# Kernel tuning notes

Hardware: AMD Instinct MI355X
Metric: run time of the kernel (lower is better)

Reference implementation:

```python
import jax, jax.numpy as jnp
import numpy as np

D = 768       # input_dim / model width
H = 3072      # expert hidden width (init arg 'output_dim')
E = 8         # num_experts
K = 2         # top_k
NOISE_STD = 0.1
B, S = 2, 1024


def setup_inputs() -> dict:
    key = jax.random.key(0)
    ks = jax.random.split(key, 16)
    sd = lambda fan_in: 1.0 / np.sqrt(fan_in)
    return {
        "x": jax.random.normal(ks[0], (B, S, D), dtype=jnp.float32),
        "noise": jax.random.normal(ks[1], (B, S, E), dtype=jnp.float32),
        # router
        "Wr": jax.random.normal(ks[2], (D, E), dtype=jnp.float32) * sd(D),
        "br": jnp.zeros((E,), dtype=jnp.float32),
        # stacked expert FFNs: d -> h -> d
        "W1": jax.random.normal(ks[3], (E, D, H), dtype=jnp.float32) * sd(D),
        "b1": jnp.zeros((E, H), dtype=jnp.float32),
        "W2": jax.random.normal(ks[4], (E, H, D), dtype=jnp.float32) * sd(H),
        "b2": jnp.zeros((E, D), dtype=jnp.float32),
        # shared expert
        "Ws1": jax.random.normal(ks[5], (D, H), dtype=jnp.float32) * sd(D),
        "bs1": jnp.zeros((H,), dtype=jnp.float32),
        "Ws2": jax.random.normal(ks[6], (H, D), dtype=jnp.float32) * sd(H),
        "bs2": jnp.zeros((D,), dtype=jnp.float32),
        # mixing scalars (alpha trainable, beta frozen in torch)
        "alpha": jnp.float32(0.3),
        "beta": jnp.float32(0.7),
    }


def reference(x, noise, Wr, br, W1, b1, W2, b2, Ws1, bs1, Ws2, bs2, alpha, beta):
    b, s, d = x.shape
    xt = x.reshape(-1, d)                       # [T, D]
    nt = noise.reshape(-1, E)                   # [T, E]
    T = xt.shape[0]

    # router: noisy logits -> top-k -> softmax over selected experts only
    logits = xt @ Wr + br + NOISE_STD * nt      # [T, E]
    top_vals, top_idx = jax.lax.top_k(logits, K)  # [T, K]
    top_w = jax.nn.softmax(top_vals, axis=-1)     # softmax over -inf-masked logits == softmax over top-k
    gates = jnp.zeros((T, E), dtype=x.dtype).at[jnp.arange(T)[:, None], top_idx].set(top_w)  # [T, E], 0 elsewhere

    # experts (dense over E; non-selected contributions are zeroed by gates)
    h = jax.nn.leaky_relu(jnp.einsum('td,edh->teh', xt, W1) + b1, negative_slope=0.01)  # [T, E, H]
    y = jnp.einsum('teh,ehd->ted', h, W2) + b2                                          # [T, E, D]
    moe_out = jnp.einsum('ted,te->td', y, gates)                                        # [T, D]

    # shared expert
    sh = jax.nn.leaky_relu(xt @ Ws1 + bs1, negative_slope=0.01)
    shared_out = sh @ Ws2 + bs2                                                         # [T, D]

    w = jax.nn.softmax(jnp.stack([alpha, beta]))
    out = shared_out * w[0] + moe_out * w[1]
    return out.reshape(b, s, d)
```

## Files before the change

kernel.cpp:

```cpp
#include <hip/hip_runtime.h>
#include <hip/hip_bf16.h>
#include <cstdio>
#include <cstdint>

#define TNUM 2048
#define DDIM 768
#define HDIM 3072
#define ENUM 8

#define WAITVM(N) asm volatile("s_waitcnt vmcnt(" #N ")" ::: "memory")
#define MEMFENCE() asm volatile("" ::: "memory")

typedef __attribute__((ext_vector_type(8))) __bf16 bf16x8;
typedef __attribute__((ext_vector_type(4))) float f32x4;

__device__ __forceinline__ unsigned short f2bf(float f) {
    __bf16 h = (__bf16)f;
    unsigned short u;
    __builtin_memcpy(&u, &h, 2);
    return u;
}

__device__ __forceinline__ void async_cp16(const unsigned short* g, unsigned short* l) {
    __builtin_amdgcn_global_load_lds((const __attribute__((address_space(1))) void*)g,
                                     (__attribute__((address_space(3))) void*)l,
                                     16, 0, 0);
}

__device__ __forceinline__ void transpose_tile(const float* __restrict__ in,
                                               unsigned short* __restrict__ out,
                                               int R, int C, int c0, int r0,
                                               unsigned int* tileT32) {
    int tid = threadIdx.x;
    int l15 = tid & 15;
    int g = tid >> 4;
    int par = (g >> 1) & 1;
    int hf = g & 1;
    int cb = hf * 64 + l15 * 4;
    const float* src = in + (size_t)(r0 + (g >> 1)) * C + c0 + cb;
    float4 v[16];
    #pragma unroll
    for (int p = 0; p < 16; p++)
        v[p] = *(const float4*)(src + (size_t)p * 8 * C);
    #pragma unroll
    for (int p = 0; p < 16; p++) {
        int unit = p * 16 + g;
        unsigned int m01 = (unsigned int)f2bf(v[p].x) | ((unsigned int)f2bf(v[p].y) << 16);
        unsigned int m23 = (unsigned int)f2bf(v[p].z) | ((unsigned int)f2bf(v[p].w) << 16);
        unsigned int o01 = __shfl_xor(m01, 32);
        unsigned int o23 = __shfl_xor(m23, 32);
        unsigned int wA = par ? ((o23 & 0xffffu) | (m23 << 16))
                              : ((m01 & 0xffffu) | (o01 << 16));
        unsigned int wB = par ? ((o23 >> 16) | (m23 & 0xffff0000u))
                              : ((m01 >> 16) | (o01 & 0xffff0000u));
        int ca = cb + par * 2;
        int rp = unit >> 2;
        int cq = ca >> 2;
        int woff = 4 * (((rp >> 2) + 3 * cq) & 15) + (((rp & 3) + cq) & 3);
        tileT32[ca * 68 + woff] = wA;
        tileT32[(ca + 1) * 68 + woff] = wB;
    }
    __syncthreads();
    uint4 Wv[8];
    #pragma unroll
    for (int p = 0; p < 8; p++) {
        int cc = p * 16 + g;
        int cqp = cc >> 2;
        Wv[p] = *(const uint4*)&tileT32[cc * 68 + 4 * ((l15 + 3 * cqp) & 15)];
    }
    #pragma unroll
    for (int p = 0; p < 8; p++) {
        int cc = p * 16 + g;
        int cqp = cc >> 2;
        unsigned int a0 = Wv[p].x, a1 = Wv[p].y, a2 = Wv[p].z, a3 = Wv[p].w;
        int rsel = cqp & 3;
        if (rsel & 1) { unsigned int t = a0; a0 = a1; a1 = a2; a2 = a3; a3 = t; }
        if (rsel & 2) { unsigned int t0 = a0, t1 = a1; a0 = a2; a1 = a3; a2 = t0; a3 = t1; }
        uint4 ov; ov.x = a0; ov.y = a1; ov.z = a2; ov.w = a3;
        *(uint4*)(out + (size_t)(c0 + cc) * R + r0 + l15 * 8) = ov;
    }
}

__global__ __launch_bounds__(256, 4)
void pre_kernel(const float* __restrict__ x, const float* __restrict__ noise,
                const float* __restrict__ Wr, const float* __restrict__ br,
                const float* __restrict__ W1, const float* __restrict__ Ws1,
                const float* __restrict__ W2, const float* __restrict__ Ws2,
                unsigned short* __restrict__ W1t, unsigned short* __restrict__ Ws1t,
                unsigned short* __restrict__ W2t, unsigned short* __restrict__ Ws2t,
                unsigned short* __restrict__ xb,
                int* __restrict__ counts, int* __restrict__ list,
                int* __restrict__ inv, float* __restrict__ tokp) {
    __shared__ __align__(16) unsigned int tileT32[128 * 68];
    int b = blockIdx.x;
    if (b < 1296) {
        int m = b / 144, t = b % 144;
        const float* in       = (m < 8) ? (W1 + (size_t)m * DDIM * HDIM) : Ws1;
        unsigned short* out   = (m < 8) ? (W1t + (size_t)m * HDIM * DDIM) : Ws1t;
        transpose_tile(in, out, DDIM, HDIM, (t % 24) * 128, (t / 24) * 128, tileT32);
        return;
    }
    if (b < 2592) {
        int q = b - 1296;
        int m = q / 144, t = q % 144;
        const float* in     = (m < 8) ? (W2 + (size_t)m * HDIM * DDIM) : Ws2;
        unsigned short* out = (m < 8) ? (W2t + (size_t)m * DDIM * HDIM) : Ws2t;
        transpose_tile(in, out, HDIM, DDIM, (t % 6) * 128, (t / 6) * 128, tileT32);
        return;
    }
    if (b < 3360) {
        int i = ((b - 2592) * 256 + threadIdx.x) * 8;
        float4 a = *(const float4*)(x + i);
        float4 bb = *(const float4*)(x + i + 4);
        ushort4 lo = make_ushort4(f2bf(a.x), f2bf(a.y), f2bf(a.z), f2bf(a.w));
        ushort4 hi = make_ushort4(f2bf(bb.x), f2bf(bb.y), f2bf(bb.z), f2bf(bb.w));
        *(ushort4*)(xb + i) = lo;
        *(ushort4*)(xb + i + 4) = hi;
        return;
    }
    int lane = threadIdx.x & 63;
    int t = (b - 3360) * 4 + (threadIdx.x >> 6);
    float acc[8];
    #pragma unroll
    for (int e = 0; e < 8; e++) acc[e] = 0.f;
    #pragma unroll
    for (int i = 0; i < 12; i++) {
        int d = i * 64 + lane;
        float xv = x[t * DDIM + d];
        float4 w0 = *(const float4*)(Wr + d * 8);
        float4 w1 = *(const float4*)(Wr + d * 8 + 4);
        acc[0] += xv * w0.x; acc[1] += xv * w0.y; acc[2] += xv * w0.z; acc[3] += xv * w0.w;
        acc[4] += xv * w1.x; acc[5] += xv * w1.y; acc[6] += xv * w1.z; acc[7] += xv * w1.w;
    }
    #pragma unroll
    for (int e = 0; e < 8; e++) {
        #pragma unroll
        for (int off2 = 32; off2 >= 1; off2 >>= 1)
            acc[e] += __shfl_xor(acc[e], off2, 64);
    }
    if (lane == 0) {
        float lg[8];
        #pragma unroll
        for (int e = 0; e < 8; e++) lg[e] = acc[e] + br[e] + 0.1f * noise[t * 8 + e];
        int e0 = 0;
        #pragma unroll
        for (int e = 1; e < 8; e++) if (lg[e] > lg[e0]) e0 = e;
        int e1 = -1;
        #pragma unroll
        for (int e = 0; e < 8; e++) if (e != e0 && (e1 < 0 || lg[e] > lg[e1])) e1 = e;
        float m = fmaxf(lg[e0], lg[e1]);
        float p0 = expf(lg[e0] - m), p1 = expf(lg[e1] - m);
        float inv_s = 1.f / (p0 + p1);
        int s0 = atomicAdd(&counts[e0], 1);
        list[e0 * TNUM + s0] = t;
        int s1 = atomicAdd(&counts[e1], 1);
        list[e1 * TNUM + s1] = t;
        inv[t * 2 + 0] = (e0 << 16) | s0;
        inv[t * 2 + 1] = (e1 << 16) | s1;
        tokp[t * 2 + 0] = p0 * inv_s;
        tokp[t * 2 + 1] = p1 * inv_s;
    }
}


__global__ __launch_bounds__(256, 5)
void ffn1_kernel(const unsigned short* __restrict__ xb,
                 const unsigned short* __restrict__ W1t,
                 const unsigned short* __restrict__ Ws1t,
                 const float* __restrict__ b1, const float* __restrict__ bs1,
                 const int* __restrict__ counts, const int* __restrict__ list,
                 unsigned short* __restrict__ hbuf) {
    __shared__ __align__(16) unsigned short As[2][512 * 8];
    __shared__ __align__(16) unsigned short Bs[2][512 * 8];

    int j = blockIdx.z * 8 + blockIdx.x;
    int y = blockIdx.y;
    int mt0 = y / 12, ntl = y % 12;

    int offv[8];
    { int s = 0;
      #pragma unroll
      for (int e = 0; e < 8; e++) { offv[e] = s; s += counts[e]; } }

    int cnt, hbase, n0, mbase, ntiles;
    const unsigned short* Bmat;
    const float* bias;
    const int* lst = nullptr;
    if (j < 16) {
        int e = j >> 1, nh = j & 1;
        cnt = counts[e];
        ntiles = (cnt + 127) >> 7;
        mbase = 0;
        hbase = offv[e];
        n0 = nh * 1536 + ntl * 128;
        Bmat = W1t + (size_t)e * HDIM * DDIM;
        bias = b1 + e * HDIM;
        lst = list + e * TNUM;
    } else {
        int q = j - 16;
        int ms = q >> 1, nh = q & 1;
        mbase = ms * 512;
        ntiles = 4;
        cnt = 1 << 30;
        hbase = 2 * TNUM;
        n0 = nh * 1536 + ntl * 128;
        Bmat = Ws1t;
        bias = bs1;
    }
    if (mt0 >= ntiles) return;

    int tid = threadIdx.x;
    int w = tid >> 6, lane = tid & 63;
    int l15 = lane & 15, quad = lane >> 4;
    int wm = (w & 1) * 64, wn = (w >> 1) * 64;
    int rcA = (w & 1) * 4;
    int rcB = (w >> 1) * 4;
    const int KT = DDIM / 32;

    const unsigned short* gB[2];
    int ldsoff[2], rowl[2];
    #pragma unroll
    for (int r = 0; r < 2; r++) {
        int rc = r * 4 + w;
        rowl[r] = rc * 16 + l15;
        ldsoff[r] = rc * 512;
        gB[r] = Bmat + (size_t)(n0 + rowl[r]) * DDIM + quad * 8;
    }

    for (int mt = mt0; mt < ntiles; mt += 8) {
        int m0 = mbase + mt * 128;
        const unsigned short* gA[2];
        #pragma unroll
        for (int r = 0; r < 2; r++) {
            int row;
            if (lst) row = lst[min(m0 + rowl[r], cnt - 1)];
            else     row = m0 + rowl[r];
            gA[r] = xb + (size_t)row * DDIM + quad * 8;
        }

        f32x4 zero = {0.f, 0.f, 0.f, 0.f};
        f32x4 acc[4][4];
        #pragma unroll
        for (int i = 0; i < 4; i++)
            #pragma unroll
            for (int jj = 0; jj < 4; jj++) acc[i][jj] = zero;

        #pragma unroll
        for (int t = 0; t < 2; t++)
            #pragma unroll
            for (int r = 0; r < 2; r++) {
                async_cp16(gA[r] + t * 32, &As[t][ldsoff[r]]);
                async_cp16(gB[r] + t * 32, &Bs[t][ldsoff[r]]);
            }

        #pragma unroll 1
        for (int kt = 0; kt < KT; kt++) {
            if (kt == KT - 1) { WAITVM(0); } else { WAITVM(4); }
            __builtin_amdgcn_s_barrier();
            MEMFENCE();
            int cur = kt & 1;
            bf16x8 af[4], bv[4];
            #pragma unroll
            for (int i = 0; i < 4; i++)
                af[i] = *(const bf16x8*)&As[cur][((rcA + i) * 64 + quad * 16 + l15) * 8];
            #pragma unroll
            for (int jj = 0; jj < 4; jj++)
                bv[jj] = *(const bf16x8*)&Bs[cur][((rcB + jj) * 64 + quad * 16 + l15) * 8];
            #pragma unroll
            for (int i = 0; i < 4; i++)
                #pragma unroll
                for (int jj = 0; jj < 4; jj++)
                    acc[i][jj] = __builtin_amdgcn_mfma_f32_16x16x32_bf16(af[i], bv[jj], acc[i][jj], 0, 0, 0);
            MEMFENCE();
            __builtin_amdgcn_s_barrier();
            MEMFENCE();
            if (kt + 2 < KT) {
                int ko = (kt + 2) * 32;
                #pragma unroll
                for (int r = 0; r < 2; r++) {
                    async_cp16(gA[r] + ko, &As[cur][ldsoff[r]]);
                    async_cp16(gB[r] + ko, &Bs[cur][ldsoff[r]]);
                }
            }
        }

        #pragma unroll
        for (int i = 0; i < 4; i++) {
            int rbase = m0 + wm + i * 16 + quad * 4;
            #pragma unroll
            for (int jj = 0; jj < 4; jj++) {
                int gc = n0 + wn + jj * 16 + l15;
                float bvl = bias[gc];
                #pragma unroll
                for (int r = 0; r < 4; r++) {
                    int gr = rbase + r;
                    if (gr < cnt) {
                        float v = acc[i][jj][r] + bvl;
                        v = v > 0.f ? v : 0.01f * v;
                        hbuf[(size_t)(hbase + gr) * HDIM + gc] = f2bf(v);
                    }
                }
            }
        }
    }
}

__global__ __launch_bounds__(256, 6)
void ffn2_kernel(const unsigned short* __restrict__ hbuf,
                 const unsigned short* __restrict__ W2t,
                 const unsigned short* __restrict__ Ws2t,
                 const int* __restrict__ counts,
                 float* __restrict__ ybuf) {
    __shared__ __align__(16) unsigned short As[2][256 * 8];
    __shared__ __align__(16) unsigned short Bs[2][512 * 8];

    int j = blockIdx.z * 8 + blockIdx.x;
    int y = blockIdx.y;
    int mt0 = y / 6, ntl = y % 6;
    int n0 = ntl * 128;

    int offv[8];
    { int s = 0;
      #pragma unroll
      for (int e = 0; e < 8; e++) { offv[e] = s; s += counts[e]; } }

    int cnt, hbase, mbase, kh, ntiles;
    const unsigned short* Bmat;
    if (j < 16) {
        int e = j >> 1; kh = j & 1;
        cnt = counts[e];
        ntiles = (cnt + 63) >> 6;
        mbase = 0;
        hbase = offv[e];
        Bmat = W2t + (size_t)e * DDIM * HDIM;
    } else {
        int q = j - 16;
        int mh = q >> 1; kh = q & 1;
        mbase = mh * 512;
        ntiles = 8;
        cnt = 1 << 30;
        hbase = 2 * TNUM;
        Bmat = Ws2t;
    }
    if (mt0 >= ntiles) return;
    int kbase = kh * (HDIM / 2);

    int tid = threadIdx.x;
    int w = tid >> 6, lane = tid & 63;
    int l15 = lane & 15, quad = lane >> 4;
    int wm = (w & 1) * 32, wn = (w >> 1) * 64;
    int rcA = (w & 1) * 2;
    int rcB = (w >> 1) * 4;
    const int KT = (HDIM / 2) / 32;
    int rowl = w * 16 + l15;

    const unsigned short* gB[2];
    int ldsoffB[2];
    #pragma unroll
    for (int r = 0; r < 2; r++) {
        int rc = r * 4 + w;
        gB[r] = Bmat + (size_t)(n0 + rc * 16 + l15) * HDIM + kbase + quad * 8;
        ldsoffB[r] = rc * 512;
    }
    float* yb = ybuf + (size_t)kh * 6144 * DDIM;

    for (int mt = mt0; mt < ntiles; mt += 16) {
        int m0 = mbase + mt * 64;
        int ra = (j < 16) ? min(m0 + rowl, cnt - 1) : (m0 + rowl);
        const unsigned short* gA0 = hbuf + (size_t)(hbase + ra) * HDIM + kbase + quad * 8;

        f32x4 zero = {0.f, 0.f, 0.f, 0.f};
        f32x4 acc[2][4];
        #pragma unroll
        for (int i = 0; i < 2; i++)
            #pragma unroll
            for (int jj = 0; jj < 4; jj++) acc[i][jj] = zero;

        #pragma unroll
        for (int t = 0; t < 2; t++) {
            async_cp16(gA0 + t * 32, &As[t][w * 512]);
            #pragma unroll
            for (int r = 0; r < 2; r++) async_cp16(gB[r] + t * 32, &Bs[t][ldsoffB[r]]);
        }

        #pragma unroll 1
        for (int kt = 0; kt < KT; kt++) {
            if (kt == KT - 1) { WAITVM(0); } else { WAITVM(3); }
            __builtin_amdgcn_s_barrier();
            MEMFENCE();
            int cur = kt & 1;
            bf16x8 af[2], bv[4];
            #pragma unroll
            for (int i = 0; i < 2; i++)
                af[i] = *(const bf16x8*)&As[cur][((rcA + i) * 64 + quad * 16 + l15) * 8];
            #pragma unroll
            for (int jj = 0; jj < 4; jj++)
                bv[jj] = *(const bf16x8*)&Bs[cur][((rcB + jj) * 64 + quad * 16 + l15) * 8];
            #pragma unroll
            for (int i = 0; i < 2; i++)
                #pragma unroll
                for (int jj = 0; jj < 4; jj++)
                    acc[i][jj] = __builtin_amdgcn_mfma_f32_16x16x32_bf16(af[i], bv[jj], acc[i][jj], 0, 0, 0);
            MEMFENCE();
            __builtin_amdgcn_s_barrier();
            MEMFENCE();
            if (kt + 2 < KT) {
                int ko = (kt + 2) * 32;
                async_cp16(gA0 + ko, &As[cur][w * 512]);
                #pragma unroll
                for (int r = 0; r < 2; r++) async_cp16(gB[r] + ko, &Bs[cur][ldsoffB[r]]);
            }
        }

        #pragma unroll
        for (int i = 0; i < 2; i++) {
            int rbase = m0 + wm + i * 16 + quad * 4;
            #pragma unroll
            for (int r = 0; r < 4; r++) {
                int gr = rbase + r;
                if (gr >= cnt) continue;
                float* orow = yb + (size_t)(hbase + gr) * DDIM + n0 + wn;
                #pragma unroll
                for (int jj = 0; jj < 4; jj++)
                    orow[jj * 16 + l15] = acc[i][jj][r];
            }
        }
    }
}

__global__ void mix_kernel(const float* __restrict__ ybuf, const int* __restrict__ inv,
                           const float* __restrict__ tokp, const int* __restrict__ counts,
                           const float* __restrict__ b2, const float* __restrict__ bs2,
                           const float* __restrict__ alpha, const float* __restrict__ beta,
                           float* __restrict__ out) {
    int t = blockIdx.x;
    int c = threadIdx.x * 4;
    int offv[8];
    { int s = 0;
      #pragma unroll
      for (int e = 0; e < 8; e++) { offv[e] = s; s += counts[e]; } }
    float a = alpha[0], bsc = beta[0];
    float m = fmaxf(a, bsc);
    float ea = expf(a - m), eb = expf(bsc - m);
    float is = 1.f / (ea + eb);
    float ws = ea * is, wmx = eb * is;

    int i0 = inv[t * 2 + 0], i1 = inv[t * 2 + 1];
    int e0 = i0 >> 16, sl0 = i0 & 0xFFFF;
    int e1 = i1 >> 16, sl1 = i1 & 0xFFFF;
    float p0 = tokp[t * 2 + 0], p1 = tokp[t * 2 + 1];
    size_t rA = (size_t)(offv[e0] + sl0) * DDIM + c;
    size_t rB = (size_t)(offv[e1] + sl1) * DDIM + c;
    size_t rS = (size_t)(2 * TNUM + t) * DDIM + c;
    const float* y0 = ybuf;
    const float* y1 = ybuf + (size_t)6144 * DDIM;
    float4 vA0 = *(const float4*)(y0 + rA);
    float4 vA1 = *(const float4*)(y1 + rA);
    float4 vB0 = *(const float4*)(y0 + rB);
    float4 vB1 = *(const float4*)(y1 + rB);
    float4 vS0 = *(const float4*)(y0 + rS);
    float4 vS1 = *(const float4*)(y1 + rS);
    float4 bA = *(const float4*)(b2 + e0 * DDIM + c);
    float4 bB = *(const float4*)(b2 + e1 * DDIM + c);
    float4 bS = *(const float4*)(bs2 + c);
    float4 o;
    o.x = ws * (vS0.x + vS1.x + bS.x) + wmx * (p0 * (vA0.x + vA1.x + bA.x) + p1 * (vB0.x + vB1.x + bB.x));
    o.y = ws * (vS0.y + vS1.y + bS.y) + wmx * (p0 * (vA0.y + vA1.y + bA.y) + p1 * (vB0.y + vB1.y + bB.y));
    o.z = ws * (vS0.z + vS1.z + bS.z) + wmx * (p0 * (vA0.z + vA1.z + bA.z) + p1 * (vB0.z + vB1.z + bB.z));
    o.w = ws * (vS0.w + vS1.w + bS.w) + wmx * (p0 * (vA0.w + vA1.w + bA.w) + p1 * (vB0.w + vB1.w + bB.w));
    *(float4*)(out + (size_t)t * DDIM + c) = o;
}

extern "C" void kernel_launch(void* const* d_in, const int* in_sizes, int n_in,
                              void* d_out, int out_size, void* d_ws, size_t ws_size,
                              hipStream_t stream) {
    const float* x     = (const float*)d_in[0];
    const float* noise = (const float*)d_in[1];
    const float* Wr    = (const float*)d_in[2];
    const float* br    = (const float*)d_in[3];
    const float* W1    = (const float*)d_in[4];
    const float* b1    = (const float*)d_in[5];
    const float* W2    = (const float*)d_in[6];
    const float* b2    = (const float*)d_in[7];
    const float* Ws1   = (const float*)d_in[8];
    const float* bs1   = (const float*)d_in[9];
    const float* Ws2   = (const float*)d_in[10];
    const float* bs2   = (const float*)d_in[11];
    const float* alpha = (const float*)d_in[12];
    const float* beta  = (const float*)d_in[13];

    char* ws = (char*)d_ws;
    size_t off = 0;
    auto alloc = [&](size_t bytes) -> char* {
        char* p = ws + off;
        off = (off + bytes + 255) & ~(size_t)255;
        return p;
    };
    int*   counts = (int*)  alloc(ENUM * 4);
    int*   list   = (int*)  alloc((size_t)ENUM * TNUM * 4);
    int*   inv    = (int*)  alloc((size_t)TNUM * 2 * 4);
    float* tokp   = (float*)alloc((size_t)TNUM * 2 * 4);
    unsigned short* xb   = (unsigned short*)alloc((size_t)TNUM * DDIM * 2);
    unsigned short* W1t  = (unsigned short*)alloc((size_t)ENUM * HDIM * DDIM * 2);
    unsigned short* Ws1t = (unsigned short*)alloc((size_t)HDIM * DDIM * 2);
    unsigned short* W2t  = (unsigned short*)alloc((size_t)ENUM * DDIM * HDIM * 2);
    unsigned short* Ws2t = (unsigned short*)alloc((size_t)DDIM * HDIM * 2);
    unsigned short* hbuf = (unsigned short*)alloc((size_t)(3 * TNUM) * HDIM * 2);
    float* ybuf = (float*)W1t;
    if (off > ws_size) {
        fprintf(stderr, "kernel_launch: workspace too small (need %zu, have %zu)\n", off, ws_size);
        return;
    }

    hipMemsetAsync(counts, 0, ENUM * 4, stream);

    pre_kernel<<<dim3(3872), dim3(256), 0, stream>>>(x, noise, Wr, br, W1, Ws1, W2, Ws2,
                                                     W1t, Ws1t, W2t, Ws2t, xb,
                                                     counts, list, inv, tokp);
    ffn1_kernel<<<dim3(8, 96, 3), dim3(256), 0, stream>>>(xb, W1t, Ws1t, b1, bs1, counts, list, hbuf);
    ffn2_kernel<<<dim3(8, 96, 3), dim3(256), 0, stream>>>(hbuf, W2t, Ws2t, counts, ybuf);
    mix_kernel<<<dim3(TNUM), dim3(192), 0, stream>>>(ybuf, inv, tokp, counts, b2, bs2,
                                                     alpha, beta, (float*)d_out);
}
```

Before: 483.6 us.

## Fuse W1 fp32-to-bf16 conversion into ffn1 and drop the separate W1 transpose pass

The pre-kernel no longer transposes and converts W1/Ws1 to bf16. Instead ffn1 reads the fp32 weights directly with register loads, converts them to bf16 and packs pairs of k-rows into a swizzled LDS layout, then rotates the words on read to rebuild MFMA B fragments. This removes a full write and re-read of about 40 MB of bf16 weights. The cost is fp32 weight reads inside the GEMM (twice the bytes), conversion ALU in the main loop, and a single-stage B prefetch. The grid shapes, per-block tile loops and launch bounds of ffn1 and ffn2 change, and ybuf gets its own workspace allocation.

Result: faster. 444.0 us (-8.2%).

```diff
diff --git a/kernel.cpp b/kernel.cpp
--- a/kernel.cpp
+++ b/kernel.cpp
@@ -9,6 +9,7 @@
 #define ENUM 8
 
 #define WAITVM(N) asm volatile("s_waitcnt vmcnt(" #N ")" ::: "memory")
+#define WAITLGKM() asm volatile("s_waitcnt lgkmcnt(0)" ::: "memory")
 #define MEMFENCE() asm volatile("" ::: "memory")
 
 typedef __attribute__((ext_vector_type(8))) __bf16 bf16x8;
@@ -84,9 +85,7 @@
 __global__ __launch_bounds__(256, 4)
 void pre_kernel(const float* __restrict__ x, const float* __restrict__ noise,
                 const float* __restrict__ Wr, const float* __restrict__ br,
-                const float* __restrict__ W1, const float* __restrict__ Ws1,
                 const float* __restrict__ W2, const float* __restrict__ Ws2,
-                unsigned short* __restrict__ W1t, unsigned short* __restrict__ Ws1t,
                 unsigned short* __restrict__ W2t, unsigned short* __restrict__ Ws2t,
                 unsigned short* __restrict__ xb,
                 int* __restrict__ counts, int* __restrict__ list,
@@ -95,21 +94,13 @@
     int b = blockIdx.x;
     if (b < 1296) {
         int m = b / 144, t = b % 144;
-        const float* in       = (m < 8) ? (W1 + (size_t)m * DDIM * HDIM) : Ws1;
-        unsigned short* out   = (m < 8) ? (W1t + (size_t)m * HDIM * DDIM) : Ws1t;
-        transpose_tile(in, out, DDIM, HDIM, (t % 24) * 128, (t / 24) * 128, tileT32);
-        return;
-    }
-    if (b < 2592) {
-        int q = b - 1296;
-        int m = q / 144, t = q % 144;
         const float* in     = (m < 8) ? (W2 + (size_t)m * HDIM * DDIM) : Ws2;
         unsigned short* out = (m < 8) ? (W2t + (size_t)m * DDIM * HDIM) : Ws2t;
         transpose_tile(in, out, HDIM, DDIM, (t % 6) * 128, (t / 6) * 128, tileT32);
         return;
     }
-    if (b < 3360) {
-        int i = ((b - 2592) * 256 + threadIdx.x) * 8;
+    if (b < 2064) {
+        int i = ((b - 1296) * 256 + threadIdx.x) * 8;
         float4 a = *(const float4*)(x + i);
         float4 bb = *(const float4*)(x + i + 4);
         ushort4 lo = make_ushort4(f2bf(a.x), f2bf(a.y), f2bf(a.z), f2bf(a.w));
@@ -119,7 +110,7 @@
         return;
     }
     int lane = threadIdx.x & 63;
-    int t = (b - 3360) * 4 + (threadIdx.x >> 6);
+    int t = (b - 2064) * 4 + (threadIdx.x >> 6);
     float acc[8];
     #pragma unroll
     for (int e = 0; e < 8; e++) acc[e] = 0.f;
@@ -162,20 +153,19 @@
     }
 }
 
-
-__global__ __launch_bounds__(256, 5)
+__global__ __launch_bounds__(256, 3)
 void ffn1_kernel(const unsigned short* __restrict__ xb,
-                 const unsigned short* __restrict__ W1t,
-                 const unsigned short* __restrict__ Ws1t,
+                 const float* __restrict__ W1,
+                 const float* __restrict__ Ws1,
                  const float* __restrict__ b1, const float* __restrict__ bs1,
                  const int* __restrict__ counts, const int* __restrict__ list,
                  unsigned short* __restrict__ hbuf) {
     __shared__ __align__(16) unsigned short As[2][512 * 8];
-    __shared__ __align__(16) unsigned short Bs[2][512 * 8];
+    __shared__ __align__(16) unsigned int Bs32[2048];
 
     int j = blockIdx.z * 8 + blockIdx.x;
     int y = blockIdx.y;
-    int mt0 = y / 12, ntl = y % 12;
+    int mt0 = y / 6, ntl = y % 6;
 
     int offv[8];
     { int s = 0;
@@ -183,28 +173,28 @@
       for (int e = 0; e < 8; e++) { offv[e] = s; s += counts[e]; } }
 
     int cnt, hbase, n0, mbase, ntiles;
-    const unsigned short* Bmat;
+    const float* Bf;
     const float* bias;
     const int* lst = nullptr;
-    if (j < 16) {
-        int e = j >> 1, nh = j & 1;
+    if (j < 32) {
+        int e = j >> 2, nq = j & 3;
         cnt = counts[e];
         ntiles = (cnt + 127) >> 7;
         mbase = 0;
         hbase = offv[e];
-        n0 = nh * 1536 + ntl * 128;
-        Bmat = W1t + (size_t)e * HDIM * DDIM;
+        n0 = nq * 768 + ntl * 128;
+        Bf = W1 + (size_t)e * DDIM * HDIM;
         bias = b1 + e * HDIM;
         lst = list + e * TNUM;
     } else {
-        int q = j - 16;
-        int ms = q >> 1, nh = q & 1;
-        mbase = ms * 512;
-        ntiles = 4;
+        int q = j - 32;
+        int ms = q >> 2, nq = q & 3;
+        mbase = ms * 1024;
+        ntiles = 8;
         cnt = 1 << 30;
         hbase = 2 * TNUM;
-        n0 = nh * 1536 + ntl * 128;
-        Bmat = Ws1t;
+        n0 = nq * 768 + ntl * 128;
+        Bf = Ws1;
         bias = bs1;
     }
     if (mt0 >= ntiles) return;
@@ -217,17 +207,21 @@
     int rcB = (w >> 1) * 4;
     const int KT = DDIM / 32;
 
-    const unsigned short* gB[2];
+    int l31 = tid & 31;
+    int rp0 = tid >> 5;
+    int nlh = l31 >> 2;
+    int nll4 = (l31 & 3) * 4;
+    int c4 = l31 * 4;
+
     int ldsoff[2], rowl[2];
     #pragma unroll
     for (int r = 0; r < 2; r++) {
         int rc = r * 4 + w;
         rowl[r] = rc * 16 + l15;
         ldsoff[r] = rc * 512;
-        gB[r] = Bmat + (size_t)(n0 + rowl[r]) * DDIM + quad * 8;
-    }
-
-    for (int mt = mt0; mt < ntiles; mt += 8) {
+    }
+
+    for (int mt = mt0; mt < ntiles; mt += 4) {
         int m0 = mbase + mt * 128;
         const unsigned short* gA[2];
         #pragma unroll
@@ -246,26 +240,60 @@
             for (int jj = 0; jj < 4; jj++) acc[i][jj] = zero;
 
         #pragma unroll
-        for (int t = 0; t < 2; t++)
-            #pragma unroll
-            for (int r = 0; r < 2; r++) {
-                async_cp16(gA[r] + t * 32, &As[t][ldsoff[r]]);
-                async_cp16(gB[r] + t * 32, &Bs[t][ldsoff[r]]);
-            }
+        for (int r = 0; r < 2; r++) async_cp16(gA[r], &As[0][ldsoff[r]]);
+        float4 Ba[2], Bb[2];
+        #pragma unroll
+        for (int p = 0; p < 2; p++) {
+            const float* bp = Bf + (size_t)(2 * (p * 8 + rp0)) * HDIM + n0 + c4;
+            Ba[p] = *(const float4*)bp;
+            Bb[p] = *(const float4*)(bp + HDIM);
+        }
 
         #pragma unroll 1
         for (int kt = 0; kt < KT; kt++) {
-            if (kt == KT - 1) { WAITVM(0); } else { WAITVM(4); }
+            int cur = kt & 1;
+            WAITVM(0);
+            #pragma unroll
+            for (int p = 0; p < 2; p++) {
+                int kp = p * 8 + rp0;
+                int gb = ((nlh * 64 + (kp >> 2) * 16 + nll4) << 2) + ((kp + nlh) & 3);
+                float4 a = Ba[p], b = Bb[p];
+                Bs32[gb + 0]  = (unsigned int)f2bf(a.x) | ((unsigned int)f2bf(b.x) << 16);
+                Bs32[gb + 4]  = (unsigned int)f2bf(a.y) | ((unsigned int)f2bf(b.y) << 16);
+                Bs32[gb + 8]  = (unsigned int)f2bf(a.z) | ((unsigned int)f2bf(b.z) << 16);
+                Bs32[gb + 12] = (unsigned int)f2bf(a.w) | ((unsigned int)f2bf(b.w) << 16);
+            }
+            if (kt + 1 < KT) {
+                int ko = (kt + 1) * 32;
+                #pragma unroll
+                for (int r = 0; r < 2; r++)
+                    async_cp16(gA[r] + ko, &As[cur ^ 1][ldsoff[r]]);
+                #pragma unroll
+                for (int p = 0; p < 2; p++) {
+                    const float* bp = Bf + (size_t)(ko + 2 * (p * 8 + rp0)) * HDIM + n0 + c4;
+                    Ba[p] = *(const float4*)bp;
+                    Bb[p] = *(const float4*)(bp + HDIM);
+                }
+            }
+            WAITLGKM();
             __builtin_amdgcn_s_barrier();
             MEMFENCE();
-            int cur = kt & 1;
             bf16x8 af[4], bv[4];
             #pragma unroll
             for (int i = 0; i < 4; i++)
                 af[i] = *(const bf16x8*)&As[cur][((rcA + i) * 64 + quad * 16 + l15) * 8];
             #pragma unroll
-            for (int jj = 0; jj < 4; jj++)
-                bv[jj] = *(const bf16x8*)&Bs[cur][((rcB + jj) * 64 + quad * 16 + l15) * 8];
+            for (int jj = 0; jj < 4; jj++) {
+                uint4 Wv = *(const uint4*)&Bs32[((rcB + jj) * 64 + quad * 16 + l15) << 2];
+                unsigned int s0 = Wv.x, s1 = Wv.y, s2 = Wv.z, s3 = Wv.w;
+                unsigned int t0, t1, t2, t3;
+                if (jj == 0)      { t0 = s0; t1 = s1; t2 = s2; t3 = s3; }
+                else if (jj == 1) { t0 = s1; t1 = s2; t2 = s3; t3 = s0; }
+                else if (jj == 2) { t0 = s2; t1 = s3; t2 = s0; t3 = s1; }
+                else              { t0 = s3; t1 = s0; t2 = s1; t3 = s2; }
+                uint4 L; L.x = t0; L.y = t1; L.z = t2; L.w = t3;
+                __builtin_memcpy(&bv[jj], &L, 16);
+            }
             #pragma unroll
             for (int i = 0; i < 4; i++)
                 #pragma unroll
@@ -274,14 +302,6 @@
             MEMFENCE();
             __builtin_amdgcn_s_barrier();
             MEMFENCE();
-            if (kt + 2 < KT) {
-                int ko = (kt + 2) * 32;
-                #pragma unroll
-                for (int r = 0; r < 2; r++) {
-                    async_cp16(gA[r] + ko, &As[cur][ldsoff[r]]);
-                    async_cp16(gB[r] + ko, &Bs[cur][ldsoff[r]]);
-                }
-            }
         }
 
         #pragma unroll
@@ -305,7 +325,7 @@
     }
 }
 
-__global__ __launch_bounds__(256, 6)
+__global__ __launch_bounds__(256, 4)
 void ffn2_kernel(const unsigned short* __restrict__ hbuf,
                  const unsigned short* __restrict__ W2t,
                  const unsigned short* __restrict__ Ws2t,
@@ -364,7 +384,7 @@
     }
     float* yb = ybuf + (size_t)kh * 6144 * DDIM;
 
-    for (int mt = mt0; mt < ntiles; mt += 16) {
+    for (int mt = mt0; mt < ntiles; mt += 8) {
         int m0 = mbase + mt * 64;
         int ra = (j < 16) ? min(m0 + rowl, cnt - 1) : (m0 + rowl);
         const unsigned short* gA0 = hbuf + (size_t)(hbase + ra) * HDIM + kbase + quad * 8;
@@ -501,12 +521,10 @@
     int*   inv    = (int*)  alloc((size_t)TNUM * 2 * 4);
     float* tokp   = (float*)alloc((size_t)TNUM * 2 * 4);
     unsigned short* xb   = (unsigned short*)alloc((size_t)TNUM * DDIM * 2);
-    unsigned short* W1t  = (unsigned short*)alloc((size_t)ENUM * HDIM * DDIM * 2);
-    unsigned short* Ws1t = (unsigned short*)alloc((size_t)HDIM * DDIM * 2);
+    float* ybuf          = (float*)alloc((size_t)2 * 6144 * DDIM * 4);
     unsigned short* W2t  = (unsigned short*)alloc((size_t)ENUM * DDIM * HDIM * 2);
     unsigned short* Ws2t = (unsigned short*)alloc((size_t)DDIM * HDIM * 2);
     unsigned short* hbuf = (unsigned short*)alloc((size_t)(3 * TNUM) * HDIM * 2);
-    float* ybuf = (float*)W1t;
     if (off > ws_size) {
         fprintf(stderr, "kernel_launch: workspace too small (need %zu, have %zu)\n", off, ws_size);
         return;
@@ -514,11 +532,10 @@
 
     hipMemsetAsync(counts, 0, ENUM * 4, stream);
 
-    pre_kernel<<<dim3(3872), dim3(256), 0, stream>>>(x, noise, Wr, br, W1, Ws1, W2, Ws2,
-                                                     W1t, Ws1t, W2t, Ws2t, xb,
-                                                     counts, list, inv, tokp);
-    ffn1_kernel<<<dim3(8, 96, 3), dim3(256), 0, stream>>>(xb, W1t, Ws1t, b1, bs1, counts, list, hbuf);
-    ffn2_kernel<<<dim3(8, 96, 3), dim3(256), 0, stream>>>(hbuf, W2t, Ws2t, counts, ybuf);
+    pre_kernel<<<dim3(2576), dim3(256), 0, stream>>>(x, noise, Wr, br, W2, Ws2,
+                                                     W2t, Ws2t, xb, counts, list, inv, tokp);
+    ffn1_kernel<<<dim3(8, 24, 5), dim3(256), 0, stream>>>(xb, W1, Ws1, b1, bs1, counts, list, hbuf);
+    ffn2_kernel<<<dim3(8, 48, 3), dim3(256), 0, stream>>>(hbuf, W2t, Ws2t, counts, ybuf);
     mix_kernel<<<dim3(TNUM), dim3(192), 0, stream>>>(ybuf, inv, tokp, counts, b2, bs2,
                                                      alpha, beta, (float*)d_out);
 }
```
